# Performance work log

Hardware: AMD Instinct MI355X
Metric: run time of the kernel (lower is better)

## Reference

```python
import jax, jax.numpy as jnp
import numpy as np

SCALE = 1000.0
NEG = -1000000000.0
B, S, T, E, H = 64, 512, 96, 256, 512  # batch, src_len, trg_len, embed_dim, hidden_dim
ENC_DIM = 2 * H


def setup_inputs() -> dict:
    key = jax.random.key(0)
    def rn(i, shape):
        return jax.random.normal(jax.random.fold_in(key, i), shape, jnp.float32) / np.sqrt(shape[-1])
    inp = {}
    inp["src"] = jax.random.uniform(jax.random.fold_in(key, 100), (B, S), jnp.float32, 50.0, 1500.0)
    src_len = jax.random.randint(jax.random.fold_in(key, 101), (B,), S // 2, S + 1)
    inp["src_mask"] = (jnp.arange(S)[None, :] < src_len[:, None]).astype(jnp.int32)
    trg = jax.random.uniform(jax.random.fold_in(key, 102), (B, T), jnp.float32, 50.0, 1500.0)
    inp["trg"] = trg.at[:, 0].set(0.0)  # position 0 is the start sentinel
    trg_len = jax.random.randint(jax.random.fold_in(key, 103), (B,), T // 2, T + 1)
    inp["trg_mask"] = (jnp.arange(T)[None, :] < trg_len[:, None]).astype(jnp.int32)
    shapes = {
        "enc_proj_W": (E, 1), "enc_proj_b": (E,),
        "enc_Wih_f": (4 * H, E), "enc_Whh_f": (4 * H, H), "enc_bih_f": (4 * H,), "enc_bhh_f": (4 * H,),
        "enc_Wih_b": (4 * H, E), "enc_Whh_b": (4 * H, H), "enc_bih_b": (4 * H,), "enc_bhh_b": (4 * H,),
        "fc_h_W": (H, 2 * H), "fc_h_b": (H,), "fc_c_W": (H, 2 * H), "fc_c_b": (H,),
        "dec_proj_W": (E, 1), "dec_proj_b": (E,),
        "attn_Wenc": (H, ENC_DIM), "attn_Wdec": (H, H), "attn_v": (1, H),
        "dec_Wih": (4 * H, E + ENC_DIM), "dec_Whh": (4 * H, H), "dec_bih": (4 * H,), "dec_bhh": (4 * H,),
        "val_W": (1, H + ENC_DIM + E), "val_b": (1,),
        "stop_W": (1, H + ENC_DIM + E), "stop_b": (1,),
    }
    for i, (name, shp) in enumerate(shapes.items()):
        inp[name] = rn(i, shp)
    return inp


def _lstm_scan(x_tbe, m_tb1, Wih, Whh, bih, bhh, reverse):
    # Mask-gated LSTM scan == pack_padded_sequence semantics (padding at end):
    # state is frozen and outputs zeroed at padded steps; reverse=True gives the
    # backward direction of the bidirectional encoder.
    b, h = x_tbe.shape[1], Whh.shape[1]
    init = (jnp.zeros((b, h), x_tbe.dtype), jnp.zeros((b, h), x_tbe.dtype))
    bias = bih + bhh
    def step(carry, xm):
        hprev, cprev = carry
        xt, m = xm
        gates = xt @ Wih.T + hprev @ Whh.T + bias  # [B,4H], torch gate order i,f,g,o
        i, f, g, o = jnp.split(gates, 4, axis=-1)
        c_new = jax.nn.sigmoid(f) * cprev + jax.nn.sigmoid(i) * jnp.tanh(g)
        h_new = jax.nn.sigmoid(o) * jnp.tanh(c_new)
        hn = jnp.where(m, h_new, hprev)
        cn = jnp.where(m, c_new, cprev)
        return (hn, cn), jnp.where(m, h_new, 0.0)
    (hT, cT), outs = jax.lax.scan(step, init, (x_tbe, m_tb1), reverse=reverse)
    return outs, hT, cT


def _forward(src, trg, enc_proj_W, enc_proj_b, enc_Wih_f, enc_Whh_f, enc_bih_f, enc_bhh_f, enc_Wih_b, enc_Whh_b, enc_bih_b, enc_bhh_b, fc_h_W, fc_h_b, fc_c_W, fc_c_b, dec_proj_W, dec_proj_b, attn_Wenc, attn_Wdec, attn_v, dec_Wih, dec_Whh, dec_bih, dec_bhh, val_W, val_b, stop_W, stop_b, src_mask, trg_mask):
    src_norm = src / SCALE
    # ---- encoder (bidirectional, n_layers=1, dropout inactive in eval) ----
    emb = src_norm[..., None] * enc_proj_W[:, 0] + enc_proj_b  # Linear(1,E) -> [B,S,E]
    emb_t = jnp.transpose(emb, (1, 0, 2))                      # [S,B,E] time-major
    m_t = (src_mask.T > 0)[..., None]                          # [S,B,1]
    out_f, hF, cF = _lstm_scan(emb_t, m_t, enc_Wih_f, enc_Whh_f, enc_bih_f, enc_bhh_f, False)
    out_b, hB, cB = _lstm_scan(emb_t, m_t, enc_Wih_b, enc_Whh_b, enc_bih_b, enc_bhh_b, True)
    enc_outputs = jnp.transpose(jnp.concatenate([out_f, out_b], -1), (1, 0, 2))  # [B,S,2H]
    hidden = jnp.tanh(jnp.concatenate([hF, hB], -1) @ fc_h_W.T + fc_h_b)  # [B,H]
    cell = jnp.tanh(jnp.concatenate([cF, cB], -1) @ fc_c_W.T + fc_c_b)    # [B,H]
    # ---- decoder loop (full teacher forcing, ratio=1.0) ----
    eh = enc_outputs @ attn_Wenc.T  # [B,S,H], loop-invariant (same math, hoisted)
    valid = src_mask > 0            # [B,S]
    dec_bias = dec_bih + dec_bhh
    def dec_step(carry, x_t):
        h, c = carry
        energy = jnp.tanh((h @ attn_Wdec.T)[:, None, :] + eh)  # [B,S,H]
        scores = jnp.where(valid, energy @ attn_v[0], NEG)     # [B,S]
        w = jax.nn.softmax(scores, axis=1)
        context = jnp.einsum('bs,bse->be', w, enc_outputs)     # [B,2H]
        e = x_t[:, None] * dec_proj_W[:, 0] + dec_proj_b       # [B,E]
        gates = jnp.concatenate([e, context], -1) @ dec_Wih.T + h @ dec_Whh.T + dec_bias
        i, f, g, o = jnp.split(gates, 4, axis=-1)
        c_new = jax.nn.sigmoid(f) * c + jax.nn.sigmoid(i) * jnp.tanh(g)
        h_new = jax.nn.sigmoid(o) * jnp.tanh(c_new)
        feat = jnp.concatenate([h_new, context, e], -1)        # [B, H+2H+E]
        pv = feat @ val_W[0] + val_b[0]
        sl = feat @ stop_W[0] + stop_b[0]
        return (h_new, c_new), (pv * SCALE, sl)
    dec_in = (trg[:, :-1] / SCALE).T  # [T-1,B]: inputs for steps t=1..trg_len-1
    _, (pred_values, stop_logits) = jax.lax.scan(dec_step, (hidden, cell), dec_in)
    return pred_values.T, stop_logits.T  # each [B, T-1]


def reference(src, src_mask, trg, trg_mask, enc_proj_W, enc_proj_b, enc_Wih_f, enc_Whh_f, enc_bih_f, enc_bhh_f, enc_Wih_b, enc_Whh_b, enc_bih_b, enc_bhh_b, fc_h_W, fc_h_b, fc_c_W, fc_c_b, dec_proj_W, dec_proj_b, attn_Wenc, attn_Wdec, attn_v, dec_Wih, dec_Whh, dec_bih, dec_bhh, val_W, val_b, stop_W, stop_b):
    return _forward(src, trg, enc_proj_W, enc_proj_b, enc_Wih_f, enc_Whh_f, enc_bih_f, enc_bhh_f, enc_Wih_b, enc_Whh_b, enc_bih_b, enc_bhh_b, fc_h_W, fc_h_b, fc_c_W, fc_c_b, dec_proj_W, dec_proj_b, attn_Wenc, attn_Wdec, attn_v, dec_Wih, dec_Whh, dec_bih, dec_bhh, val_W, val_b, stop_W, stop_b, src_mask, trg_mask)
```

## Files before the change

### kernel.cpp

```cpp
#include <hip/hip_runtime.h>
#include <hip/hip_bf16.h>

#define AGENT __HIP_MEMORY_SCOPE_AGENT

typedef float f32x4 __attribute__((ext_vector_type(4)));
typedef short short8 __attribute__((ext_vector_type(8)));
union V16 { f32x4 f; short8 s; };


__device__ __forceinline__ float sigm(float x){ return 1.f/(1.f+__expf(-x)); }
__device__ __forceinline__ float tanhfast(float x){
  float ax = fabsf(x);
  float e = __expf(-2.f*ax);
  float r = (1.f-e)/(1.f+e);
  return copysignf(r, x);
}
__device__ __forceinline__ float dot4(float4 a, float4 b){
  return fmaf(a.x,b.x, fmaf(a.y,b.y, fmaf(a.z,b.z, a.w*b.w)));
}
__device__ __forceinline__ unsigned short bfbits(float x){
  return __bfloat16_as_ushort(__float2bfloat16(x));
}
__device__ __forceinline__ float bfu2f(unsigned short u){
  union{unsigned v; float f;} x; x.v = ((unsigned)u)<<16; return x.f;
}

__global__ void __launch_bounds__(256) precompute(
  const float* __restrict__ Wenc,
  const float* __restrict__ Wihf, const float* __restrict__ epW, const float* __restrict__ epb,
  const float* __restrict__ bihf, const float* __restrict__ bhhf,
  const float* __restrict__ Wihb, const float* __restrict__ bihb, const float* __restrict__ bhhb,
  const float* __restrict__ dWih, const float* __restrict__ dpW, const float* __restrict__ dpb,
  const float* __restrict__ dbih, const float* __restrict__ dbhh,
  const float* __restrict__ valW, const float* __restrict__ valb,
  const float* __restrict__ stopW, const float* __restrict__ stopb,
  float* __restrict__ PQ, float* __restrict__ WT, float* __restrict__ hc)
{
  const int idx = blockIdx.x*256 + threadIdx.x;
  if (idx < 524288){
    const int j = idx >> 9, n = idx & 511;
    WT[idx] = Wenc[(size_t)n*1024 + j];
  } else if (idx < 524288 + 6*2048){
    const int q = idx - 524288;
    const int set = q >> 11, j = q & 2047;
    const float* row; const float* vec; float add = 0.f;
    switch(set){
      case 0: row = Wihf + (size_t)j*256; vec = epW; break;
      case 1: row = Wihf + (size_t)j*256; vec = epb; add = bihf[j]+bhhf[j]; break;
      case 2: row = Wihb + (size_t)j*256; vec = epW; break;
      case 3: row = Wihb + (size_t)j*256; vec = epb; add = bihb[j]+bhhb[j]; break;
      case 4: row = dWih + (size_t)j*1280; vec = dpW; break;
      default: row = dWih + (size_t)j*1280; vec = dpb; add = dbih[j]+dbhh[j]; break;
    }
    float a = add;
    for (int e=0;e<256;e++) a = fmaf(row[e], vec[e], a);
    PQ[set*2048 + j] = a;
  } else if (idx < 524288 + 6*2048 + 4){
    const int q = idx - (524288 + 6*2048);
    const float* wrow = (q<2) ? valW : stopW;
    const float* vec  = (q&1) ? dpb : dpW;
    float a = (q&1) ? ((q<2)? valb[0] : stopb[0]) : 0.f;
    for (int e=0;e<256;e++) a = fmaf(wrow[1536+e], vec[e], a);
    hc[q] = a;
  }
}

__global__ void __launch_bounds__(512) wconv(
  const float* __restrict__ Whhf, const float* __restrict__ Whhb,
  const float* __restrict__ dWih, const float* __restrict__ dWhh,
  const float* __restrict__ Wdec, const float* __restrict__ Wenc,
  unsigned short* __restrict__ Wbf, unsigned short* __restrict__ Wcat,
  unsigned short* __restrict__ Wdecb, unsigned short* __restrict__ Wencb)
{
  const int i = blockIdx.x*512 + threadIdx.x;
  if (i < 2097152){
    const float v = (i < 1048576) ? Whhf[i] : Whhb[i-1048576];
    Wbf[i] = bfbits(v);
  } else if (i < 2097152+3145728){
    const int q = i - 2097152;
    const int r = q/1536, k = q - r*1536;
    const float v = (k<1024) ? dWih[(size_t)r*1280 + 256 + k] : dWhh[(size_t)r*512 + (k-1024)];
    Wcat[q] = bfbits(v);
  } else if (i < 2097152+3145728+262144){
    const int q = i - (2097152+3145728);
    Wdecb[q] = bfbits(Wdec[q]);
  } else if (i < 2097152+3145728+262144+524288){
    const int q = i - (2097152+3145728+262144);
    Wencb[q] = bfbits(Wenc[q]);
  }
}

__global__ void __launch_bounds__(512) enc_mfma(
    const float* __restrict__ src, const int* __restrict__ smask,
    const unsigned short* __restrict__ Wbf,
    const float* __restrict__ PQ,
    unsigned short* __restrict__ hbuf,
    float* __restrict__ hfin,
    float* __restrict__ cf, float* __restrict__ cb,
    __hip_bfloat16* __restrict__ enc,
    unsigned* __restrict__ eflag)
{
  __shared__ float hlds[16*256];
  __shared__ float red[4*64*4];
  __shared__ float gbuf[4*256];
  __shared__ alignas(16) unsigned short hstage[256];
  __shared__ alignas(16) unsigned short estage[256];

  const int tid = threadIdx.x;
  const int bid = blockIdx.x;
  const int dir = bid>>7, bhalf = (bid>>5)&3, us = bid&31;
  const int b0 = bhalf*16;
  const int gbase = bid & ~31;
  const int wv = tid>>6, lane = tid&63;
  const int nt = wv&3, kh = wv>>2;
  const int rowb = lane&15;

  short8 bfr[8];
  {
    const int g = nt*512 + us*16 + (lane&15);
    const unsigned short* wp = Wbf + ((size_t)dir*2048 + g)*512 + kh*256 + (lane>>4)*8;
    #pragma unroll
    for (int kt=0;kt<8;kt++) bfr[kt] = *(const short8*)(wp + kt*32);
  }

  float p0=0,p1=0,p2=0,p3=0,q0=0,q1=0,q2=0,q3=0;
  float creg = 0.f, hprev = 0.f;
  int bg = 0, ug = 0;
  if (tid < 256){
    bg = b0 + (tid>>4);
    ug = us*16 + (tid&15);
    const float* P = PQ + dir*4096; const float* Q = P + 2048;
    p0=P[ug]; p1=P[ug+512]; p2=P[ug+1024]; p3=P[ug+1536];
    q0=Q[ug]; q1=Q[ug+512]; q2=Q[ug+1024]; q3=Q[ug+1536];
  }

  for (int tt=0; tt<512; ++tt){
    const int t = dir ? (511-tt) : tt;
    if (tt>0){
      if (tid < 32){
        const unsigned* fp = eflag + (size_t)(gbase + tid)*32;
        unsigned v = __hip_atomic_load(fp, __ATOMIC_RELAXED, AGENT);
        while (v < (unsigned)tt){
          __builtin_amdgcn_s_sleep(1);
          v = __hip_atomic_load(fp, __ATOMIC_RELAXED, AGENT);
        }
      }
      __syncthreads();
      const int par = (tt-1)&1;
      f32x4 tmp0, tmp1;
      {
        const int f0 = tid, f1 = 512 + tid;
        const unsigned short* g0 = hbuf + (((size_t)(dir*2+par)*64 + b0 + (f0>>6))<<9) + (f0&63)*8;
        const unsigned short* g1 = hbuf + (((size_t)(dir*2+par)*64 + b0 + (f1>>6))<<9) + (f1&63)*8;
        asm volatile("global_load_dwordx4 %0, %1, off sc0 sc1" : "=v"(tmp0) : "v"(g0) : "memory");
        asm volatile("global_load_dwordx4 %0, %1, off sc0 sc1" : "=v"(tmp1) : "v"(g1) : "memory");
      }
      asm volatile("s_waitcnt vmcnt(0)" ::: "memory");
      __builtin_amdgcn_sched_barrier(0);
      {
        const int r0 = tid>>6, c0 = tid&63;
        *(f32x4*)&hlds[r0*256 + ((c0 ^ (r0&7))<<2)] = tmp0;
        const int r1 = (512+tid)>>6, c1 = tid&63;
        *(f32x4*)&hlds[r1*256 + ((c1 ^ (r1&7))<<2)] = tmp1;
      }
      __syncthreads();
    }

    f32x4 acc = {0.f,0.f,0.f,0.f};
    if (tt>0){
      #pragma unroll
      for (int kt=0; kt<8; ++kt){
        const int ch = (kh*8 + kt)*4 + (lane>>4);
        V16 a; a.f = *(const f32x4*)&hlds[rowb*256 + ((ch ^ (rowb&7))<<2)];
        acc = __builtin_amdgcn_mfma_f32_16x16x32_bf16(a.s, bfr[kt], acc, 0, 0, 0);
      }
    }
    if (kh==1) *(f32x4*)&red[(nt*64+lane)*4] = acc;
    __syncthreads();
    if (kh==0){
      const f32x4 o = *(const f32x4*)&red[(nt*64+lane)*4];
      #pragma unroll
      for (int i=0;i<4;i++){
        const int r = (lane>>4)*4 + i, c = lane&15;
        gbuf[nt*256 + r*16 + c] = acc[i] + o[i];
      }
    }
    __syncthreads();

    if (tid < 256){
      const float sx = src[bg*512+t]*0.001f;
      const int m = smask[bg*512+t];
      const float gi = gbuf[0*256+tid] + sx*p0 + q0;
      const float gf = gbuf[1*256+tid] + sx*p1 + q1;
      const float gg = gbuf[2*256+tid] + sx*p2 + q2;
      const float go = gbuf[3*256+tid] + sx*p3 + q3;
      const float cn = fmaf(sigm(gf), creg, sigm(gi)*tanhfast(gg));
      const float hn = sigm(go)*tanhfast(cn);
      const float hk = m ? hn : hprev;
      creg = m ? cn : creg;
      hprev = hk;
      hstage[tid] = bfbits(hk);
      estage[tid] = bfbits(m ? hn : 0.f);
    }
    __syncthreads();
    if (tid < 32){
      const int row = tid>>1, hw = tid&1;
      const f32x4 v = *(const f32x4*)(hstage + row*16 + hw*8);
      unsigned short* dst = hbuf + (((size_t)(dir*2+(tt&1))*64 + b0 + row)<<9) + us*16 + hw*8;
      asm volatile("global_store_dwordx4 %0, %1, off sc0 sc1" :: "v"(dst), "v"(v) : "memory");
    } else if (tid < 64){
      const int j = tid-32, row = j>>1, hw = j&1;
      const f32x4 v = *(const f32x4*)(estage + row*16 + hw*8);
      *(f32x4*)((unsigned short*)enc + ((size_t)((b0+row)*512 + t))*1024 + dir*512 + us*16 + hw*8) = v;
    }
    asm volatile("s_waitcnt vmcnt(0)" ::: "memory");
    __syncthreads();
    if (tid==0)
      __hip_atomic_store(eflag + (size_t)bid*32, (unsigned)(tt+1), __ATOMIC_RELAXED, AGENT);
  }

  if (tid < 256){
    hfin[dir*32768 + bg*512 + ug] = hprev;
    (dir ? cb : cf)[bg*512 + ug] = creg;
  }
}

__global__ void __launch_bounds__(256) fc_init(
  const float* __restrict__ hf0, const float* __restrict__ hb0,
  const float* __restrict__ cf, const float* __restrict__ cb,
  const float* __restrict__ fchW, const float* __restrict__ fchB,
  const float* __restrict__ fccW, const float* __restrict__ fccB,
  float* __restrict__ dech, float* __restrict__ decc)
{
  const int which = blockIdx.x >> 7;
  const int wid = blockIdx.x & 127;
  const int b = threadIdx.x >> 2, ul = threadIdx.x & 3;
  const int u = wid*4 + ul;
  const float* s0 = which ? cf : hf0;
  const float* s1 = which ? cb : hb0;
  const float* W = which ? fccW : fchW;
  float acc = (which ? fccB : fchB)[u];
  const float4* x0 = (const float4*)(s0 + b*512);
  const float4* x1 = (const float4*)(s1 + b*512);
  const float4* wr = (const float4*)(W + (size_t)u*1024);
  #pragma unroll 4
  for (int k=0;k<128;k++) acc += dot4(x0[k], wr[k]);
  #pragma unroll 4
  for (int k=0;k<128;k++) acc += dot4(x1[k], wr[128+k]);
  (which ? decc : dech)[b*512+u] = tanhfast(acc);
}

__global__ void __launch_bounds__(256) eh_mfma(
  const unsigned short* __restrict__ enc,
  const unsigned short* __restrict__ Wencb,
  unsigned short* __restrict__ eh2)
{
  const int b = blockIdx.x>>6, st = (blockIdx.x>>3)&7, nt0 = blockIdx.x&7;
  const int wv = threadIdx.x>>6, lane = threadIdx.x&63;
  const int sA = st*64 + wv*16 + (lane&15);
  const int kb = (lane>>4)*8;
  const unsigned short* ap  = enc + ((size_t)(b*512 + sA))*1024 + kb;
  const unsigned short* bp0 = Wencb + ((size_t)(nt0*64 + (lane&15)))*1024 + kb;
  f32x4 acc[4] = {{0,0,0,0},{0,0,0,0},{0,0,0,0},{0,0,0,0}};
  for (int k0=0; k0<1024; k0+=32){
    V16 a; a.f = *(const f32x4*)(ap + k0);
    #pragma unroll
    for (int nt=0; nt<4; ++nt){
      V16 bb; bb.f = *(const f32x4*)(bp0 + (size_t)nt*16*1024 + k0);
      acc[nt] = __builtin_amdgcn_mfma_f32_16x16x32_bf16(a.s, bb.s, acc[nt], 0, 0, 0);
    }
  }
  const int sO = st*64 + wv*16 + (lane>>4)*4;
  const int col = lane&15;
  #pragma unroll
  for (int nt=0; nt<4; ++nt){
    #pragma unroll
    for (int i=0;i<4;i++){
      eh2[((size_t)(b*512 + sO + i))*512 + nt0*64 + nt*16 + col] = bfbits(acc[nt][i]);
    }
  }
}

__global__ void __launch_bounds__(256) enc_tr(
  const unsigned short* __restrict__ enc, unsigned short* __restrict__ encT2)
{
  __shared__ unsigned short tl[64][80];
  const int b = blockIdx.x>>7, st = (blockIdx.x>>4)&7, jt = blockIdx.x&15;
  const int r = threadIdx.x>>2, q = threadIdx.x&3;
  const unsigned short* src = enc + ((size_t)(b*512 + st*64 + r))*1024 + jt*64 + q*16;
  *(short8*)&tl[r][q*16]   = *(const short8*)src;
  *(short8*)&tl[r][q*16+8] = *(const short8*)(src+8);
  __syncthreads();
  unsigned short tmp[16];
  #pragma unroll
  for (int e=0;e<16;e++) tmp[e] = tl[q*16+e][r];
  unsigned short* dst = encT2 + ((size_t)(b*1024 + jt*64 + r))*512 + st*64 + q*16;
  *(short8*)dst     = *(short8*)&tmp[0];
  *(short8*)(dst+8) = *(short8*)&tmp[8];
}

template<int NG>
__device__ __forceinline__ void gbar(unsigned* gctr, unsigned* root, int grp, unsigned gen){
  asm volatile("s_waitcnt vmcnt(0)" ::: "memory");
  __syncthreads();
  if (threadIdx.x==0){
    const unsigned old = __hip_atomic_fetch_add(gctr + grp*32, 1u, __ATOMIC_RELAXED, AGENT);
    if (old == gen*16u - 1u)
      __hip_atomic_fetch_add(root, 1u, __ATOMIC_RELAXED, AGENT);
    while (__hip_atomic_load(root, __ATOMIC_RELAXED, AGENT) < gen*(unsigned)NG)
      __builtin_amdgcn_s_sleep(1);
  }
  __syncthreads();
}
template<int NB>
__device__ __forceinline__ void mbar(unsigned* mc, unsigned mgen){
  asm volatile("s_waitcnt vmcnt(0)" ::: "memory");
  __syncthreads();
  if (threadIdx.x==0){
    __hip_atomic_fetch_add(mc, 1u, __ATOMIC_RELAXED, AGENT);
    while (__hip_atomic_load(mc, __ATOMIC_RELAXED, AGENT) < mgen*(unsigned)NB)
      __builtin_amdgcn_s_sleep(1);
  }
  __syncthreads();
}

__device__ __forceinline__ void fgbar(unsigned* aflag, unsigned gen){
  asm volatile("s_waitcnt vmcnt(0)" ::: "memory");
  __syncthreads();
  if (threadIdx.x==0)
    __hip_atomic_store(aflag + (size_t)blockIdx.x*32, gen, __ATOMIC_RELAXED, AGENT);
  {
    unsigned v = __hip_atomic_load(aflag + (size_t)threadIdx.x*32, __ATOMIC_RELAXED, AGENT);
    while (v < gen){
      __builtin_amdgcn_s_sleep(2);
      v = __hip_atomic_load(aflag + (size_t)threadIdx.x*32, __ATOMIC_RELAXED, AGENT);
    }
  }
  __syncthreads();
}
__device__ __forceinline__ void fmbar(unsigned* mflag, int b, int oct, unsigned gen){
  asm volatile("s_waitcnt vmcnt(0)" ::: "memory");
  __syncthreads();
  if (threadIdx.x==0)
    __hip_atomic_store(mflag + (size_t)(b*8+oct)*32, gen, __ATOMIC_RELAXED, AGENT);
  if (threadIdx.x < 8){
    unsigned v = __hip_atomic_load(mflag + (size_t)(b*8+(int)threadIdx.x)*32, __ATOMIC_RELAXED, AGENT);
    while (v < gen){
      __builtin_amdgcn_s_sleep(1);
      v = __hip_atomic_load(mflag + (size_t)(b*8+(int)threadIdx.x)*32, __ATOMIC_RELAXED, AGENT);
    }
  }
  __syncthreads();
}

__global__ void __launch_bounds__(512) dec_fused256(
  const float* __restrict__ trg, const int* __restrict__ smask,
  const float* __restrict__ attnv,
  const unsigned short* __restrict__ eh2,
  const unsigned short* __restrict__ encT2,
  const unsigned short* __restrict__ Wcat,
  const unsigned short* __restrict__ Wdecb,
  const float* __restrict__ PQd, const float* __restrict__ hc,
  const float* __restrict__ valW, const float* __restrict__ stopW,
  const float* __restrict__ dech0, const float* __restrict__ decc0,
  float* __restrict__ scorep, float* __restrict__ ctxf,
  unsigned short* __restrict__ xbuf, float* __restrict__ gates,
  float* __restrict__ hcur, float* __restrict__ out,
  unsigned* __restrict__ gctr, unsigned* __restrict__ root, unsigned* __restrict__ mctr,
  unsigned* __restrict__ aflag, unsigned* __restrict__ mflag)
{
  __shared__ alignas(16) float redl[8192];
  __shared__ float vlds[512];
  __shared__ float hldsa[512];
  __shared__ float adhl[128];
  __shared__ float wlds[512];
  const int tid = threadIdx.x;
  const int bid = blockIdx.x;
  const int b = bid>>2, quad = bid&3;
  const int grp = bid>>4;
  const int lane = tid&63, wv = tid>>6;
  unsigned* mc = mctr + b*32;
  unsigned g = 0, m = 0;
  (void)aflag; (void)mflag;

  vlds[tid] = attnv[tid];

  short8 gw[6];
  if (bid < 128){
    const int n = bid*16 + (lane&15);
    const unsigned short* wp = Wcat + (size_t)n*1536 + wv*192 + (lane>>4)*8;
    #pragma unroll
    for (int ks=0;ks<6;ks++) gw[ks] = *(const short8*)(wp + ks*32);
  }

  const bool isb = (quad==0);
  float hr=0.f, cr=0.f;
  float pqi=0,pqf=0,pqg=0,pqo=0, qqi=0,qqf=0,qqg=0,qqo=0;
  float vwh=0,vwc0=0,vwc1=0, swh=0,swc0=0,swc1=0;
  if (isb){
    hr = dech0[b*512+tid]; cr = decc0[b*512+tid];
    pqi = PQd[tid];      pqf = PQd[512+tid];      pqg = PQd[1024+tid];      pqo = PQd[1536+tid];
    qqi = PQd[2048+tid]; qqf = PQd[2048+512+tid]; qqg = PQd[2048+1024+tid]; qqo = PQd[2048+1536+tid];
    vwh = valW[tid]; vwc0 = valW[512+tid]; vwc1 = valW[1024+tid];
    swh = stopW[tid]; swc0 = stopW[512+tid]; swc1 = stopW[1024+tid];
  }

  if (isb){
    const unsigned hb16 = (unsigned)bfbits(hr);
    unsigned short* xp = xbuf + b*1536 + 1024 + tid;
    asm volatile("global_store_short %0, %1, off sc0 sc1" :: "v"(xp), "v"(hb16) : "memory");
    float* hp = hcur + b*512 + tid;
    asm volatile("global_store_dword %0, %1, off sc0 sc1" :: "v"(hp), "v"(hr) : "memory");
  }
  ++m; mbar<4>(mc, m);

  for (int t=0; t<95; ++t){
    {
      float hv; const float* hp = hcur + b*512 + tid;
      asm volatile("global_load_dword %0, %1, off sc0 sc1\ns_waitcnt vmcnt(0)" : "=v"(hv) : "v"(hp) : "memory");
      hldsa[tid] = hv;
      __syncthreads();
      {
        const int jl = tid>>2, uc = tid&3;
        const unsigned short* wp = Wdecb + (size_t)(quad*128 + jl)*512 + uc*128;
        float a = 0.f;
        #pragma unroll
        for (int i=0;i<16;i++){
          const short8 w8 = *(const short8*)(wp + i*8);
          #pragma unroll
          for (int e=0;e<8;e++)
            a = fmaf(hldsa[uc*128 + i*8 + e], bfu2f((unsigned short)w8[e]), a);
        }
        redl[tid] = a;
      }
      __syncthreads();
      if (tid < 128)
        adhl[tid] = redl[tid*4] + redl[tid*4+1] + redl[tid*4+2] + redl[tid*4+3];
      __syncthreads();
      {
        const unsigned short* ep = eh2 + ((size_t)(b*512 + tid))*512 + quad*128;
        float part = 0.f;
        #pragma unroll
        for (int i=0;i<16;i++){
          const short8 e8 = *(const short8*)(ep + i*8);
          #pragma unroll
          for (int e=0;e<8;e++){
            const int n = i*8 + e;
            part = fmaf(vlds[quad*128+n], tanhfast(adhl[n] + bfu2f((unsigned short)e8[e])), part);
          }
        }
        float* sp = scorep + (size_t)bid*512 + tid;
        asm volatile("global_store_dword %0, %1, off sc0 sc1" :: "v"(sp), "v"(part) : "memory");
      }
    }
    ++m; mbar<4>(mc, m);

    {
      float pa, pb, pc, pd;
      const float* pp = scorep + (size_t)(b*4)*512 + tid;
      asm volatile("global_load_dword %0, %1, off sc0 sc1" : "=v"(pa) : "v"(pp) : "memory");
      asm volatile("global_load_dword %0, %1, off sc0 sc1" : "=v"(pb) : "v"(pp+512) : "memory");
      asm volatile("global_load_dword %0, %1, off sc0 sc1" : "=v"(pc) : "v"(pp+1024) : "memory");
      asm volatile("global_load_dword %0, %1, off sc0 sc1" : "=v"(pd) : "v"(pp+1536) : "memory");
      asm volatile("s_waitcnt vmcnt(0)" ::: "memory");
      __builtin_amdgcn_sched_barrier(0);
      float s0 = (pa+pb)+(pc+pd);
      s0 = smask[b*512+tid] ? s0 : -1.0e9f;
      redl[512+tid] = s0;
      __syncthreads();
      for (int off=256; off>0; off>>=1){
        if (tid<off) redl[512+tid] = fmaxf(redl[512+tid], redl[512+tid+off]);
        __syncthreads();
      }
      const float mx = redl[512];
      __syncthreads();
      const float e = __expf(s0 - mx);
      redl[512+tid] = e;
      __syncthreads();
      for (int off=256; off>0; off>>=1){
        if (tid<off) redl[512+tid] += redl[512+tid+off];
        __syncthreads();
      }
      const float Z = redl[512];
      __syncthreads();
      wlds[tid] = e / Z;
      __syncthreads();
      {
        const int jj = tid>>1, sh = tid&1;
        const unsigned short* cp = encT2 + ((size_t)(b*1024 + quad*256 + jj))*512 + sh*256;
        float c = 0.f;
        #pragma unroll
        for (int i=0;i<32;i++){
          const short8 c8 = *(const short8*)(cp + i*8);
          #pragma unroll
          for (int e2=0;e2<8;e2++)
            c = fmaf(wlds[sh*256 + i*8 + e2], bfu2f((unsigned short)c8[e2]), c);
        }
        redl[tid] = c;
      }
      __syncthreads();
      if (tid < 256){
        const float cv = redl[tid*2] + redl[tid*2+1];
        const int j = quad*256 + tid;
        float* cp2 = ctxf + b*1024 + j;
        asm volatile("global_store_dword %0, %1, off sc0 sc1" :: "v"(cp2), "v"(cv) : "memory");
        const unsigned cb16 = (unsigned)bfbits(cv);
        unsigned short* xp = xbuf + b*1536 + j;
        asm volatile("global_store_short %0, %1, off sc0 sc1" :: "v"(xp), "v"(cb16) : "memory");
      }
    }
    ++g; gbar<16>(gctr, root, grp, g);

    if (bid < 128){
      f32x4 av[2][6];
      f32x4 acc[4] = {{0,0,0,0},{0,0,0,0},{0,0,0,0},{0,0,0,0}};
      {
        const unsigned short* xp0 = xbuf + (size_t)(lane&15)*1536 + wv*192 + (lane>>4)*8;
        #pragma unroll
        for (int ks=0;ks<6;ks++){
          const unsigned short* p = xp0 + ks*32;
          asm volatile("global_load_dwordx4 %0, %1, off sc0 sc1" : "=v"(av[0][ks]) : "v"(p) : "memory");
        }
      }
      #pragma unroll
      for (int mt=0; mt<4; ++mt){
        if (mt<3){
          const unsigned short* xpn = xbuf + (size_t)((mt+1)*16 + (lane&15))*1536 + wv*192 + (lane>>4)*8;
          #pragma unroll
          for (int ks=0;ks<6;ks++){
            const unsigned short* p = xpn + ks*32;
            asm volatile("global_load_dwordx4 %0, %1, off sc0 sc1" : "=v"(av[(mt+1)&1][ks]) : "v"(p) : "memory");
          }
          asm volatile("s_waitcnt vmcnt(6)" ::: "memory");
        } else {
          asm volatile("s_waitcnt vmcnt(0)" ::: "memory");
        }
        __builtin_amdgcn_sched_barrier(0);
        #pragma unroll
        for (int ks=0;ks<6;ks++){
          V16 a; a.f = av[mt&1][ks];
          acc[mt] = __builtin_amdgcn_mfma_f32_16x16x32_bf16(a.s, gw[ks], acc[mt], 0, 0, 0);
        }
      }
      #pragma unroll
      for (int mt=0; mt<4; ++mt)
        *(f32x4*)&redl[wv*1024 + lane*16 + mt*4] = acc[mt];
    }
    __syncthreads();
    if (bid < 128){
      #pragma unroll
      for (int h2=0; h2<2; ++h2){
        const int o = h2*512 + tid;
        const int ob = o>>4, col = o&15;
        const int mt = ob>>4, row = ob&15;
        const int base = (((row>>2)<<4) | col)*16 + mt*4 + (row&3);
        float gsum = 0.f;
        #pragma unroll
        for (int w2=0; w2<8; ++w2) gsum += redl[w2*1024 + base];
        float* gp = gates + ob*2048 + bid*16 + col;
        asm volatile("global_store_dword %0, %1, off sc0 sc1" :: "v"(gp), "v"(gsum) : "memory");
      }
    }
    ++g; gbar<16>(gctr, root, grp, g);

    if (isb){
      float g4[4], c0v, c1v;
      {
        const float* gp = gates + b*2048 + tid;
        const float* cp = ctxf + b*1024 + tid;
        asm volatile("global_load_dword %0, %1, off sc0 sc1" : "=v"(g4[0]) : "v"(gp) : "memory");
        asm volatile("global_load_dword %0, %1, off sc0 sc1" : "=v"(g4[1]) : "v"(gp+512) : "memory");
        asm volatile("global_load_dword %0, %1, off sc0 sc1" : "=v"(g4[2]) : "v"(gp+1024) : "memory");
        asm volatile("global_load_dword %0, %1, off sc0 sc1" : "=v"(g4[3]) : "v"(gp+1536) : "memory");
        asm volatile("global_load_dword %0, %1, off sc0 sc1" : "=v"(c0v) : "v"(cp) : "memory");
        asm volatile("global_load_dword %0, %1, off sc0 sc1" : "=v"(c1v) : "v"(cp+512) : "memory");
        asm volatile("s_waitcnt vmcnt(0)" ::: "memory");
        __builtin_amdgcn_sched_barrier(0);
      }
      const float x = trg[b*96 + t]*0.001f;
      const float gi = g4[0] + x*pqi + qqi;
      const float gf = g4[1] + x*pqf + qqf;
      const float gg = g4[2] + x*pqg + qqg;
      const float go = g4[3] + x*pqo + qqo;
      const float cn = fmaf(sigm(gf), cr, sigm(gi)*tanhfast(gg));
      const float hn = sigm(go)*tanhfast(cn);
      cr = cn; hr = hn;
      const unsigned hb16 = (unsigned)bfbits(hn);
      unsigned short* xp = xbuf + b*1536 + 1024 + tid;
      asm volatile("global_store_short %0, %1, off sc0 sc1" :: "v"(xp), "v"(hb16) : "memory");
      float* hp = hcur + b*512 + tid;
      asm volatile("global_store_dword %0, %1, off sc0 sc1" :: "v"(hp), "v"(hn) : "memory");
      redl[512+tid]  = fmaf(hn, vwh, fmaf(c0v, vwc0, c1v*vwc1));
      redl[1024+tid] = fmaf(hn, swh, fmaf(c0v, swc0, c1v*swc1));
      __syncthreads();
      for (int off=256; off>0; off>>=1){
        if (tid<off){ redl[512+tid]+=redl[512+tid+off]; redl[1024+tid]+=redl[1024+tid+off]; }
        __syncthreads();
      }
      if (tid==0){
        out[b*95 + t] = (redl[512] + x*hc[0] + hc[1])*1000.f;
        out[6080 + b*95 + t] = redl[1024] + x*hc[2] + hc[3];
      }
    }
    ++m; mbar<4>(mc, m);
  }
}

__global__ void __launch_bounds__(512, 4) dec_fused512(
  const float* __restrict__ trg, const int* __restrict__ smask,
  const float* __restrict__ attnv,
  const unsigned short* __restrict__ eh2,
  const unsigned short* __restrict__ encT2,
  const unsigned short* __restrict__ Wcat,
  const unsigned short* __restrict__ Wdecb,
  const float* __restrict__ PQd, const float* __restrict__ hc,
  const float* __restrict__ valW, const float* __restrict__ stopW,
  const float* __restrict__ dech0, const float* __restrict__ decc0,
  float* __restrict__ scorep, float* __restrict__ ctxf,
  unsigned short* __restrict__ xbuf, float* __restrict__ gates,
  float* __restrict__ hcur, float* __restrict__ out,
  unsigned* __restrict__ gctr, unsigned* __restrict__ root, unsigned* __restrict__ mctr,
  unsigned* __restrict__ aflag, unsigned* __restrict__ mflag)
{
  __shared__ unsigned short eh2l[32768];
  __shared__ alignas(16) float redl[2048];
  __shared__ float vlds[512];
  __shared__ float hl[512];
  __shared__ float adhl[64];
  __shared__ int slen_sh;
  const int tid = threadIdx.x;
  const int bid = blockIdx.x;
  const int b = bid>>3, oct = bid&7;
  const int lane = tid&63, wv = tid>>6;
  unsigned g = 0, m = 0;
  (void)gctr; (void)root; (void)mctr; (void)hcur;

  vlds[tid] = attnv[tid];

  redl[tid] = (float)smask[b*512+tid];
  __syncthreads();
  for (int off=256; off>0; off>>=1){
    if (tid<off) redl[tid] += redl[tid+off];
    __syncthreads();
  }
  if (tid==0) slen_sh = (int)(redl[0]+0.5f);
  __syncthreads();
  const int slen = slen_sh;
  const int nch = (slen + 127) >> 7;

  {
    const unsigned short* ep = eh2 + ((size_t)(b*512 + tid))*512 + oct*64;
    short8 r8[8];
    #pragma unroll
    for (int i=0;i<8;i++) r8[i] = *(const short8*)(ep + i*8);
    #pragma unroll
    for (int i=0;i<8;i++)
      #pragma unroll
      for (int e=0;e<8;e++)
        eh2l[(i*8+e)*512 + tid] = (unsigned short)r8[i][e];
  }

  short8 gw[6];
  if (bid < 128){
    const int n = bid*16 + (lane&15);
    const unsigned short* wp = Wcat + (size_t)n*1536 + wv*192 + (lane>>4)*8;
    #pragma unroll
    for (int ks=0;ks<6;ks++) gw[ks] = *(const short8*)(wp + ks*32);
  }

  const bool isb = (oct==0);
  float cr = decc0[b*512+tid];
  const float pqi = PQd[tid],      pqf = PQd[512+tid],      pqg = PQd[1024+tid],      pqo = PQd[1536+tid];
  const float qqi = PQd[2048+tid], qqf = PQd[2048+512+tid], qqg = PQd[2048+1024+tid], qqo = PQd[2048+1536+tid];
  float vwh=0,vwc0=0,vwc1=0, swh=0,swc0=0,swc1=0;
  if (isb){
    vwh = valW[tid]; vwc0 = valW[512+tid]; vwc1 = valW[1024+tid];
    swh = stopW[tid]; swc0 = stopW[512+tid]; swc1 = stopW[1024+tid];
  }

  {
    const float h0 = dech0[b*512+tid];
    hl[tid] = h0;
    if (isb){
      const unsigned hb16 = (unsigned)bfbits(h0);
      unsigned short* xp = xbuf + b*1536 + 1024 + tid;
      asm volatile("global_store_short %0, %1, off sc0 sc1" :: "v"(xp), "v"(hb16) : "memory");
    }
  }
  __syncthreads();

  for (int t=0; t<95; ++t){
    {
      {
        const int jl = tid>>3, uc = tid&7;
        const unsigned short* wp = Wdecb + (size_t)(oct*64 + jl)*512 + uc*64;
        float a = 0.f;
        #pragma unroll
        for (int i=0;i<8;i++){
          const short8 w8 = *(const short8*)(wp + i*8);
          #pragma unroll
          for (int e=0;e<8;e++)
            a = fmaf(hl[uc*64 + i*8 + e], bfu2f((unsigned short)w8[e]), a);
        }
        redl[tid] = a;
      }
      __syncthreads();
      if (tid < 64){
        float s8 = 0.f;
        #pragma unroll
        for (int i=0;i<8;i++) s8 += redl[tid*8+i];
        adhl[tid] = s8;
      }
      __syncthreads();
      {
        float part = 0.f;
        #pragma unroll 8
        for (int n=0;n<64;++n)
          part = fmaf(vlds[oct*64+n], tanhfast(adhl[n] + bfu2f(eh2l[n*512 + tid])), part);
        float* sp = scorep + (size_t)bid*512 + tid;
        asm volatile("global_store_dword %0, %1, off sc0 sc1" :: "v"(sp), "v"(part) : "memory");
      }
    }
    ++m; fmbar(mflag, b, oct, m);

    {
      float ps[8];
      const float* pp = scorep + (size_t)(b*8)*512 + tid;
      #pragma unroll
      for (int i=0;i<8;i++){
        const float* p = pp + i*512;
        asm volatile("global_load_dword %0, %1, off sc0 sc1" : "=v"(ps[i]) : "v"(p) : "memory");
      }
      const int jj = tid>>2, sh = tid&3;
      const bool act = (sh < nch);
      const int she = act ? sh : 0;
      const unsigned short* cp = encT2 + ((size_t)(b*1024 + oct*128 + jj))*512 + she*128;
      f32x4 pre[8];
      #pragma unroll
      for (int i=0;i<8;i++){
        const unsigned short* p = cp + i*8;
        asm volatile("global_load_dwordx4 %0, %1, off" : "=v"(pre[i]) : "v"(p) : "memory");
      }
      asm volatile("s_waitcnt vmcnt(8)" ::: "memory");
      __builtin_amdgcn_sched_barrier(0);
      float s0 = ((ps[0]+ps[1])+(ps[2]+ps[3]))+((ps[4]+ps[5])+(ps[6]+ps[7]));
      s0 = (tid < slen) ? s0 : -1.0e9f;
      redl[512+tid] = s0;
      __syncthreads();
      for (int off=256; off>0; off>>=1){
        if (tid<off) redl[512+tid] = fmaxf(redl[512+tid], redl[512+tid+off]);
        __syncthreads();
      }
      const float mx = redl[512];
      __syncthreads();
      const float e = __expf(s0 - mx);
      redl[512+tid] = e;
      __syncthreads();
      for (int off=256; off>0; off>>=1){
        if (tid<off) redl[512+tid] += redl[512+tid+off];
        __syncthreads();
      }
      const float Z = redl[512];
      __syncthreads();
      redl[1024+tid] = e / Z;
      __syncthreads();
      float c = 0.f;
      asm volatile("s_waitcnt vmcnt(0)" ::: "memory");
      __builtin_amdgcn_sched_barrier(0);
      #pragma unroll
      for (int i=0;i<8;i++){
        V16 x; x.f = pre[i];
        #pragma unroll
        for (int e2=0;e2<8;e2++)
          c = fmaf(redl[1024 + she*128 + i*8 + e2], bfu2f((unsigned short)x.s[e2]), c);
      }
      #pragma unroll
      for (int i=8;i<16;i++){
        const short8 c8 = *(const short8*)(cp + i*8);
        #pragma unroll
        for (int e2=0;e2<8;e2++)
          c = fmaf(redl[1024 + she*128 + i*8 + e2], bfu2f((unsigned short)c8[e2]), c);
      }
      c = act ? c : 0.f;
      redl[tid] = c;
      __syncthreads();
      if (tid < 128){
        const float cv = redl[tid*4] + redl[tid*4+1] + redl[tid*4+2] + redl[tid*4+3];
        const int j = oct*128 + tid;
        float* cp2 = ctxf + b*1024 + j;
        asm volatile("global_store_dword %0, %1, off sc0 sc1" :: "v"(cp2), "v"(cv) : "memory");
        const unsigned cb16 = (unsigned)bfbits(cv);
        unsigned short* xp = xbuf + b*1536 + j;
        asm volatile("global_store_short %0, %1, off sc0 sc1" :: "v"(xp), "v"(cb16) : "memory");
      }
    }
    ++g; fgbar(aflag, g);

    redl[tid] = 0.f; redl[512+tid] = 0.f;
    __syncthreads();
    if (bid < 128){
      f32x4 av[2][6];
      f32x4 acc[4] = {{0,0,0,0},{0,0,0,0},{0,0,0,0},{0,0,0,0}};
      {
        const unsigned short* xp0 = xbuf + (size_t)(lane&15)*1536 + wv*192 + (lane>>4)*8;
        #pragma unroll
        for (int ks=0;ks<6;ks++){
          const unsigned short* p = xp0 + ks*32;
          asm volatile("global_load_dwordx4 %0, %1, off sc0 sc1" : "=v"(av[0][ks]) : "v"(p) : "memory");
        }
      }
      #pragma unroll
      for (int mt=0; mt<4; ++mt){
        if (mt<3){
          const unsigned short* xpn = xbuf + (size_t)((mt+1)*16 + (lane&15))*1536 + wv*192 + (lane>>4)*8;
          #pragma unroll
          for (int ks=0;ks<6;ks++){
            const unsigned short* p = xpn + ks*32;
            asm volatile("global_load_dwordx4 %0, %1, off sc0 sc1" : "=v"(av[(mt+1)&1][ks]) : "v"(p) : "memory");
          }
          asm volatile("s_waitcnt vmcnt(6)" ::: "memory");
        } else {
          asm volatile("s_waitcnt vmcnt(0)" ::: "memory");
        }
        __builtin_amdgcn_sched_barrier(0);
        #pragma unroll
        for (int ks=0;ks<6;ks++){
          V16 a; a.f = av[mt&1][ks];
          acc[mt] = __builtin_amdgcn_mfma_f32_16x16x32_bf16(a.s, gw[ks], acc[mt], 0, 0, 0);
        }
      }
      #pragma unroll
      for (int mt=0; mt<4; ++mt)
        #pragma unroll
        for (int i=0;i<4;i++){
          const int r = (lane>>4)*4 + i, cc = lane&15;
          atomicAdd(&redl[(mt*16 + r)*16 + cc], acc[mt][i]);
        }
    }
    __syncthreads();
    if (bid < 128){
      #pragma unroll
      for (int h2=0; h2<2; ++h2){
        const int o = h2*512 + tid;
        const int ob = o>>4, col = o&15;
        const float gsum = redl[o];
        float* gp = gates + ob*2048 + bid*16 + col;
        asm volatile("global_store_dword %0, %1, off sc0 sc1" :: "v"(gp), "v"(gsum) : "memory");
      }
    }
    ++g; fgbar(aflag, g);

    {
      float g4[4], c0v = 0.f, c1v = 0.f;
      {
        const float* gp = gates + b*2048 + tid;
        asm volatile("global_load_dword %0, %1, off sc0 sc1" : "=v"(g4[0]) : "v"(gp) : "memory");
        asm volatile("global_load_dword %0, %1, off sc0 sc1" : "=v"(g4[1]) : "v"(gp+512) : "memory");
        asm volatile("global_load_dword %0, %1, off sc0 sc1" : "=v"(g4[2]) : "v"(gp+1024) : "memory");
        asm volatile("global_load_dword %0, %1, off sc0 sc1" : "=v"(g4[3]) : "v"(gp+1536) : "memory");
        if (isb){
          const float* cp = ctxf + b*1024 + tid;
          asm volatile("global_load_dword %0, %1, off sc0 sc1" : "=v"(c0v) : "v"(cp) : "memory");
          asm volatile("global_load_dword %0, %1, off sc0 sc1" : "=v"(c1v) : "v"(cp+512) : "memory");
        }
        asm volatile("s_waitcnt vmcnt(0)" ::: "memory");
        __builtin_amdgcn_sched_barrier(0);
      }
      const float x = trg[b*96 + t]*0.001f;
      const float gi = g4[0] + x*pqi + qqi;
      const float gf = g4[1] + x*pqf + qqf;
      const float gg = g4[2] + x*pqg + qqg;
      const float go = g4[3] + x*pqo + qqo;
      const float cn = fmaf(sigm(gf), cr, sigm(gi)*tanhfast(gg));
      const float hn = sigm(go)*tanhfast(cn);
      cr = cn;
      __syncthreads();
      hl[tid] = hn;
      if (isb){
        const unsigned hb16 = (unsigned)bfbits(hn);
        unsigned short* xp = xbuf + b*1536 + 1024 + tid;
        asm volatile("global_store_short %0, %1, off sc0 sc1" :: "v"(xp), "v"(hb16) : "memory");
        redl[512+tid]  = fmaf(hn, vwh, fmaf(c0v, vwc0, c1v*vwc1));
        redl[1024+tid] = fmaf(hn, swh, fmaf(c0v, swc0, c1v*swc1));
        __syncthreads();
        for (int off=256; off>0; off>>=1){
          if (tid<off){ redl[512+tid]+=redl[512+tid+off]; redl[1024+tid]+=redl[1024+tid+off]; }
          __syncthreads();
        }
        if (tid==0){
          out[b*95 + t] = (redl[512] + x*hc[0] + hc[1])*1000.f;
          out[6080 + b*95 + t] = redl[1024] + x*hc[2] + hc[3];
        }
      }
      __syncthreads();
    }
  }
}

extern "C" void kernel_launch(void* const* d_in, const int* in_sizes, int n_in,
                              void* d_out, int out_size, void* d_ws, size_t ws_size,
                              hipStream_t stream)
{
  (void)in_sizes; (void)n_in; (void)out_size; (void)ws_size;
  const float* src   = (const float*)d_in[0];
  const int*   smask = (const int*)  d_in[1];
  const float* trg   = (const float*)d_in[2];
  const float* epW   = (const float*)d_in[4];
  const float* epb   = (const float*)d_in[5];
  const float* Wihf  = (const float*)d_in[6];
  const float* Whhf  = (const float*)d_in[7];
  const float* bihf  = (const float*)d_in[8];
  const float* bhhf  = (const float*)d_in[9];
  const float* Wihb  = (const float*)d_in[10];
  const float* Whhb  = (const float*)d_in[11];
  const float* bihb  = (const float*)d_in[12];
  const float* bhhb  = (const float*)d_in[13];
  const float* fchW  = (const float*)d_in[14];
  const float* fchB  = (const float*)d_in[15];
  const float* fccW  = (const float*)d_in[16];
  const float* fccB  = (const float*)d_in[17];
  const float* dpW   = (const float*)d_in[18];
  const float* dpb   = (const float*)d_in[19];
  const float* Wenc  = (const float*)d_in[20];
  const float* Wdec  = (const float*)d_in[21];
  const float* attnv = (const float*)d_in[22];
  const float* dWih  = (const float*)d_in[23];
  const float* dWhh  = (const float*)d_in[24];
  const float* dbih  = (const float*)d_in[25];
  const float* dbhh  = (const float*)d_in[26];
  const float* valW  = (const float*)d_in[27];
  const float* valb  = (const float*)d_in[28];
  const float* stopW = (const float*)d_in[29];
  const float* stopb = (const float*)d_in[30];
  float* out = (float*)d_out;

  char* ws = (char*)d_ws;
  size_t off = 0;
  auto take = [&](size_t nbytes) -> char* {
    char* p = ws + off;
    off += (nbytes + 255) & ~(size_t)255;
    return p;
  };
  unsigned short* enc   = (unsigned short*)take((size_t)64*512*1024*2);
  unsigned short* eh2   = (unsigned short*)take((size_t)64*512*512*2);
  unsigned short* encT2 = (unsigned short*)take((size_t)64*1024*512*2);
  unsigned short* hbuf  = (unsigned short*)take(2*2*64*512*2);
  unsigned short* Wbf   = (unsigned short*)take((size_t)2*2048*512*2);
  unsigned short* Wcat  = (unsigned short*)take((size_t)2048*1536*2);
  unsigned short* Wdecb = (unsigned short*)take(512*512*2);
  unsigned short* Wencb = (unsigned short*)take(512*1024*2);
  float* WT    = (float*)take((size_t)1024*512*4);
  float* hfin  = (float*)take(2*64*512*4);
  float* cf    = (float*)take(64*512*4);
  float* cb    = (float*)take(64*512*4);
  float* PQ    = (float*)take(6*2048*4);
  float* dech0 = (float*)take(64*512*4);
  float* decc0 = (float*)take(64*512*4);
  float* scorep= (float*)take(512*512*4);
  float* ctxf  = (float*)take(64*1024*4);
  unsigned short* xbuf = (unsigned short*)take(64*1536*2);
  float* gates = (float*)take(64*2048*4);
  float* hcur  = (float*)take(64*512*4);
  float* hc    = (float*)take(256);
  unsigned* cnt  = (unsigned*)take(1024);
  unsigned* gctr = (unsigned*)take(4096);
  unsigned* root = (unsigned*)take(256);
  unsigned* mctr = (unsigned*)take(8192);
  unsigned* aflag = (unsigned*)take(65536);
  unsigned* mflag = (unsigned*)take(65536);
  unsigned* eflag = (unsigned*)take(32768);
  float* PQd = PQ + 8192;
  (void)hipMemsetAsync(cnt, 0, 1024+4096+256+8192+65536+65536+32768, stream);

  precompute<<<2097, 256, 0, stream>>>(Wenc, Wihf, epW, epb, bihf, bhhf, Wihb, bihb, bhhb,
                                       dWih, dpW, dpb, dbih, dbhh, valW, valb, stopW, stopb,
                                       PQ, WT, hc);
  wconv<<<11776, 512, 0, stream>>>(Whhf, Whhb, dWih, dWhh, Wdec, Wenc, Wbf, Wcat, Wdecb, Wencb);

  {
    void* args[] = { (void*)&src, (void*)&smask, (void*)&Wbf, (void*)&PQ,
                     (void*)&hbuf, (void*)&hfin, (void*)&cf, (void*)&cb, (void*)&enc, (void*)&eflag };
    (void)hipLaunchCooperativeKernel((void*)enc_mfma, dim3(256), dim3(512), args, 0, stream);
  }

  {
    const float* hfF = hfin;
    const float* hbF = hfin + 32768;
    fc_init<<<256, 256, 0, stream>>>(hfF, hbF, cf, cb, fchW, fchB, fccW, fccB, dech0, decc0);
  }
  eh_mfma<<<4096, 256, 0, stream>>>(enc, Wencb, eh2);
  enc_tr<<<8192, 256, 0, stream>>>(enc, encT2);

  {
    void* args[] = { (void*)&trg, (void*)&smask, (void*)&attnv,
                     (void*)&eh2, (void*)&encT2, (void*)&Wcat, (void*)&Wdecb,
                     (void*)&PQd, (void*)&hc, (void*)&valW, (void*)&stopW,
                     (void*)&dech0, (void*)&decc0,
                     (void*)&scorep, (void*)&ctxf,
                     (void*)&xbuf, (void*)&gates, (void*)&hcur, (void*)&out,
                     (void*)&gctr, (void*)&root, (void*)&mctr,
                     (void*)&aflag, (void*)&mflag };
    int nb2 = 0;
    (void)hipOccupancyMaxActiveBlocksPerMultiprocessor(&nb2, dec_fused512, 512, 0);
    hipError_t e512 = hipErrorUnknown;
    if (nb2 >= 2)
      e512 = hipLaunchCooperativeKernel((void*)dec_fused512, dim3(512), dim3(512), args, 0, stream);
    if (e512 != hipSuccess)
      (void)hipLaunchCooperativeKernel((void*)dec_fused256, dim3(256), dim3(512), args, 0, stream);
  }
}
```

Before: 7.118 ms.

## Stage decoder x-buffer through LDS and read encoder keys directly from global

Removes the 64KB per-block LDS copy of the projected encoder keys (eh2l) and instead streams them from global memory with vector loads inside the attention-score loop. The freed LDS is reused as a padded staging buffer: each 16-row tile of xbuf is loaded cooperatively with coalesced loads, written to LDS, and then read as MFMA A-operands. This replaces the per-lane strided, double-buffered global loads. The intent is to cut LDS footprint for better occupancy and to coalesce the gate-GEMM loads. The cost is global re-reads of encoder keys every step and extra block-wide barriers per M-tile.

```diff
diff --git a/kernel.cpp b/kernel.cpp
--- a/kernel.cpp
+++ b/kernel.cpp
@@ -622,11 +622,11 @@
   unsigned* __restrict__ gctr, unsigned* __restrict__ root, unsigned* __restrict__ mctr,
   unsigned* __restrict__ aflag, unsigned* __restrict__ mflag)
 {
-  __shared__ unsigned short eh2l[32768];
   __shared__ alignas(16) float redl[2048];
   __shared__ float vlds[512];
   __shared__ float hl[512];
   __shared__ float adhl[64];
+  __shared__ alignas(16) unsigned short xstage[16*1544];
   __shared__ int slen_sh;
   const int tid = threadIdx.x;
   const int bid = blockIdx.x;
@@ -647,18 +647,6 @@
   __syncthreads();
   const int slen = slen_sh;
   const int nch = (slen + 127) >> 7;
-
-  {
-    const unsigned short* ep = eh2 + ((size_t)(b*512 + tid))*512 + oct*64;
-    short8 r8[8];
-    #pragma unroll
-    for (int i=0;i<8;i++) r8[i] = *(const short8*)(ep + i*8);
-    #pragma unroll
-    for (int i=0;i<8;i++)
-      #pragma unroll
-      for (int e=0;e<8;e++)
-        eh2l[(i*8+e)*512 + tid] = (unsigned short)r8[i][e];
-  }
 
   short8 gw[6];
   if (bid < 128){
@@ -713,10 +701,17 @@
       }
       __syncthreads();
       {
+        const unsigned short* ep = eh2 + ((size_t)(b*512 + tid))*512 + oct*64;
         float part = 0.f;
-        #pragma unroll 8
-        for (int n=0;n<64;++n)
-          part = fmaf(vlds[oct*64+n], tanhfast(adhl[n] + bfu2f(eh2l[n*512 + tid])), part);
+        #pragma unroll
+        for (int i=0;i<8;i++){
+          const short8 e8 = *(const short8*)(ep + i*8);
+          #pragma unroll
+          for (int e=0;e<8;e++){
+            const int n = i*8 + e;
+            part = fmaf(vlds[oct*64+n], tanhfast(adhl[n] + bfu2f((unsigned short)e8[e])), part);
+          }
+        }
         float* sp = scorep + (size_t)bid*512 + tid;
         asm volatile("global_store_dword %0, %1, off sc0 sc1" :: "v"(sp), "v"(part) : "memory");
       }
@@ -799,33 +794,30 @@
     redl[tid] = 0.f; redl[512+tid] = 0.f;
     __syncthreads();
     if (bid < 128){
-      f32x4 av[2][6];
       f32x4 acc[4] = {{0,0,0,0},{0,0,0,0},{0,0,0,0},{0,0,0,0}};
-      {
-        const unsigned short* xp0 = xbuf + (size_t)(lane&15)*1536 + wv*192 + (lane>>4)*8;
+      #pragma unroll
+      for (int mt=0; mt<4; ++mt){
+        __syncthreads();
+        f32x4 stg[6];
+        #pragma unroll
+        for (int c2=0;c2<6;c2++){
+          const int gci = c2*512 + tid;
+          const int row = gci/192, col = gci - row*192;
+          const unsigned short* p = xbuf + (size_t)(mt*16+row)*1536 + col*8;
+          asm volatile("global_load_dwordx4 %0, %1, off sc0 sc1" : "=v"(stg[c2]) : "v"(p) : "memory");
+        }
+        asm volatile("s_waitcnt vmcnt(0)" ::: "memory");
+        __builtin_amdgcn_sched_barrier(0);
+        #pragma unroll
+        for (int c2=0;c2<6;c2++){
+          const int gci = c2*512 + tid;
+          const int row = gci/192, col = gci - row*192;
+          *(f32x4*)&xstage[row*1544 + col*8] = stg[c2];
+        }
+        __syncthreads();
         #pragma unroll
         for (int ks=0;ks<6;ks++){
-          const unsigned short* p = xp0 + ks*32;
-          asm volatile("global_load_dwordx4 %0, %1, off sc0 sc1" : "=v"(av[0][ks]) : "v"(p) : "memory");
-        }
-      }
-      #pragma unroll
-      for (int mt=0; mt<4; ++mt){
-        if (mt<3){
-          const unsigned short* xpn = xbuf + (size_t)((mt+1)*16 + (lane&15))*1536 + wv*192 + (lane>>4)*8;
-          #pragma unroll
-          for (int ks=0;ks<6;ks++){
-            const unsigned short* p = xpn + ks*32;
-            asm volatile("global_load_dwordx4 %0, %1, off sc0 sc1" : "=v"(av[(mt+1)&1][ks]) : "v"(p) : "memory");
-          }
-          asm volatile("s_waitcnt vmcnt(6)" ::: "memory");
-        } else {
-          asm volatile("s_waitcnt vmcnt(0)" ::: "memory");
-        }
-        __builtin_amdgcn_sched_barrier(0);
-        #pragma unroll
-        for (int ks=0;ks<6;ks++){
-          V16 a; a.f = av[mt&1][ks];
+          V16 a; a.f = *(const f32x4*)&xstage[(lane&15)*1544 + wv*192 + (lane>>4)*8 + ks*32];
           acc[mt] = __builtin_amdgcn_mfma_f32_16x16x32_bf16(a.s, gw[ks], acc[mt], 0, 0, 0);
         }
       }
```

New measurement: 7.128 ms. No clear change (+0.1%).
